# Optimization experiments

Hardware: AMD Instinct MI355X
Metric: run time of the kernel (lower is better)

## Reference

```python
import jax, jax.numpy as jnp
from jax import lax
import numpy as np


def tropical_conv1d(x, w, padding, mode):
    """Tropical semiring conv1d.
    y[b,o,t] = sum_c reduce_k ( x[b,c,t+k] + w[o,c,k] )
    where reduce is min (min-plus) or max (max-plus). Zero padding like nn.Conv1d.
    x: [B, C, L], w: [O, C, K] -> y: [B, O, L + 2p - K + 1]
    """
    if padding:
        x = jnp.pad(x, ((0, 0), (0, 0), (padding, padding)))
    B, C, L = x.shape
    O, _, K = w.shape
    Lo = L - K + 1
    big = jnp.array(np.inf if mode == 'min' else -np.inf, dtype=x.dtype)
    acc0 = jnp.full((B, O, C, Lo), big, dtype=x.dtype)
    red = jnp.minimum if mode == 'min' else jnp.maximum
    wk_all = jnp.moveaxis(w, 2, 0)          # [K, O, C]
    ks = jnp.arange(K)

    def step(acc, inp):
        k, wk = inp
        xs = lax.dynamic_slice_in_dim(x, k, Lo, axis=2)      # [B, C, Lo]
        v = xs[:, None, :, :] + wk[None, :, :, None]          # [B, O, C, Lo]
        return red(acc, v), None

    acc, _ = lax.scan(step, acc0, (ks, wk_all))
    return acc.sum(axis=2)                                    # [B, O, Lo]


def avg_pool1d_2(x):
    # avg_pool1d(kernel=2, stride=2), truncating odd tail like torch
    B, C, L = x.shape
    Lh = L // 2
    return x[..., : Lh * 2].reshape(B, C, Lh, 2).mean(axis=-1)


def setup_inputs() -> dict:
    key = jax.random.key(0)
    ks = jax.random.split(key, 9)
    B, Cin, L = 64, 3, 8192
    linear_size = 32448
    s = lambda k, shape, fan: jax.random.normal(k, shape, dtype=jnp.float32) * (1.0 / np.sqrt(fan))
    return {
        'input': jax.random.normal(ks[0], (B, Cin, L), dtype=jnp.float32),
        'w1': s(ks[1], (6, Cin, 80), Cin * 80),
        'w2': s(ks[2], (16, 6, 3), 6 * 3),
        'fc1_w': s(ks[3], (120, linear_size), linear_size),
        'fc1_b': jnp.zeros((120,), jnp.float32),
        'fc2_w': s(ks[4], (84, 120), 120),
        'fc2_b': jnp.zeros((84,), jnp.float32),
        'fc3_w': s(ks[5], (10, 84), 84),
        'fc3_b': jnp.zeros((10,), jnp.float32),
    }


def reference(input, w1, w2, fc1_w, fc1_b, fc2_w, fc2_b, fc3_w, fc3_b):
    x = tropical_conv1d(input, w1, padding=2, mode='min')   # [B,6,L-75]
    x = avg_pool1d_2(x)
    x = tropical_conv1d(x, w2, padding=0, mode='max')       # [B,16,L2]
    x = avg_pool1d_2(x)
    x = x.reshape(x.shape[0], -1)                            # [B, 16*floor(L2/2)]
    x = jax.nn.relu(x @ fc1_w.T + fc1_b)
    x = jax.nn.relu(x @ fc2_w.T + fc2_b)
    return x @ fc3_w.T + fc3_b
```

## Files before the change

### kernel.cpp

```cpp
#include <hip/hip_runtime.h>

#define BB 64
#define C1 3
#define LIN 8192
#define PAD1 2
#define O1 6
#define KK1 80
#define LP1 4058

#define O2 16
#define KK2 3
#define LP2 2028

#define NFLAT 32448
#define H1 120
#define H2 84
#define NOUT 10

typedef _Float16 h2 __attribute__((ext_vector_type(2)));
typedef _Float16 f16x8 __attribute__((ext_vector_type(8)));
typedef float f32x4 __attribute__((ext_vector_type(4)));
#define BIGH ((_Float16)30000.0f)

__device__ __forceinline__ h2 bch2(float f) { return __builtin_bit_cast(h2, f); }

__global__ __launch_bounds__(256) void k_prep(const float* __restrict__ w1,
                                              float* __restrict__ whb) {
  const int idx = threadIdx.x + blockIdx.x * 256;
  if (idx >= (O1 * C1) * (KK1 / 2)) return;
  const int oc = idx / (KK1 / 2);
  const int m  = idx - oc * (KK1 / 2);
  h2 v;
  v.x = (_Float16)w1[oc * KK1 + 2 * m];
  v.y = (_Float16)w1[oc * KK1 + 2 * m + 1];
  whb[idx] = __builtin_bit_cast(float, v);
}

#define TILE2 127
#define NT12 16
#define DW12 295

__global__ __launch_bounds__(256) void k_conv12(const float* __restrict__ x,
                                                const float* __restrict__ whb,
                                                const float* __restrict__ w2,
                                                _Float16* __restrict__ p2h) {
  __shared__ float AB[C1][2 * DW12 + 2];
  __shared__ float ps[O1][256];
  __shared__ float w2s[O2 * O1 * KK2];
  const int tile = blockIdx.x;
  const int b    = blockIdx.y;
  const int pj0  = 2 * TILE2 * tile;
  const int T0   = 2 * pj0;
  const int tid  = threadIdx.x;

  for (int idx = tid; idx < O2 * O1 * KK2; idx += 256) w2s[idx] = w2[idx];
  for (int q = tid; q < C1 * DW12; q += 256) {
    const int c = q / DW12;
    const int d = q - c * DW12;
    const int E = T0 + 2 * d - PAD1;
    const float* xc = x + ((size_t)b * C1 + c) * LIN;
    float f0 = 0.f, f1 = 0.f, f2 = 0.f;
    if ((unsigned)E < LIN) f0 = xc[E];
    if ((unsigned)(E + 1) < LIN) f1 = xc[E + 1];
    if ((unsigned)(E + 2) < LIN) f2 = xc[E + 2];
    h2 A; A.x = (_Float16)f0; A.y = (_Float16)f1;
    h2 Bv; Bv.x = (_Float16)f1; Bv.y = (_Float16)f2;
    AB[c][2 * d]     = __builtin_bit_cast(float, A);
    AB[c][2 * d + 1] = __builtin_bit_cast(float, Bv);
  }
  __syncthreads();

  const int jj = tid;

  float s0 = 0.f, s1 = 0.f, s2 = 0.f, s3 = 0.f, s4 = 0.f, s5 = 0.f;

#pragma unroll
  for (int c = 0; c < C1; ++c) {
    h2 aA[O1], aB[O1];
#pragma unroll
    for (int o = 0; o < O1; ++o) {
      aA[o].x = BIGH; aA[o].y = BIGH;
      aB[o].x = BIGH; aB[o].y = BIGH;
    }
#pragma unroll 2
    for (int mc = 0; mc < 10; ++mc) {
      float4 xv0 = *(const float4*)&AB[c][2 * (jj + mc * 4)];
      float4 xv1 = *(const float4*)&AB[c][2 * (jj + mc * 4) + 4];
      h2 A0 = bch2(xv0.x), B0 = bch2(xv0.y);
      h2 A1 = bch2(xv0.z), B1 = bch2(xv0.w);
      h2 A2 = bch2(xv1.x), B2 = bch2(xv1.y);
      h2 A3 = bch2(xv1.z), B3 = bch2(xv1.w);
#pragma unroll
      for (int o = 0; o < O1; ++o) {
        float4 wq = *(const float4*)&whb[(o * C1 + c) * (KK1 / 2) + mc * 4];
        h2 w0 = bch2(wq.x), w1v = bch2(wq.y), w2v = bch2(wq.z), w3v = bch2(wq.w);
        aA[o] = __builtin_elementwise_min(aA[o], A0 + w0);
        aB[o] = __builtin_elementwise_min(aB[o], B0 + w0);
        aA[o] = __builtin_elementwise_min(aA[o], A1 + w1v);
        aB[o] = __builtin_elementwise_min(aB[o], B1 + w1v);
        aA[o] = __builtin_elementwise_min(aA[o], A2 + w2v);
        aB[o] = __builtin_elementwise_min(aB[o], B2 + w2v);
        aA[o] = __builtin_elementwise_min(aA[o], A3 + w3v);
        aB[o] = __builtin_elementwise_min(aB[o], B3 + w3v);
      }
    }
    float r[O1];
#pragma unroll
    for (int o = 0; o < O1; ++o)
      r[o] = fminf((float)aA[o].x, (float)aA[o].y) + fminf((float)aB[o].x, (float)aB[o].y);
    s0 += r[0]; s1 += r[1]; s2 += r[2]; s3 += r[3]; s4 += r[4]; s5 += r[5];
  }
  ps[0][jj] = 0.5f * s0;
  ps[1][jj] = 0.5f * s1;
  ps[2][jj] = 0.5f * s2;
  ps[3][jj] = 0.5f * s3;
  ps[4][jj] = 0.5f * s4;
  ps[5][jj] = 0.5f * s5;
  __syncthreads();

  const int j2i = tid & 127;
  const int ot  = tid >> 7;
  const int j2  = TILE2 * tile + j2i;
  if (j2i < TILE2 && j2 < LP2) {
    const int lb = 2 * j2i;
    float xv[O1][4];
#pragma unroll
    for (int c = 0; c < O1; ++c) {
      xv[c][0] = ps[c][lb];     xv[c][1] = ps[c][lb + 1];
      xv[c][2] = ps[c][lb + 2]; xv[c][3] = ps[c][lb + 3];
    }
#pragma unroll
    for (int oi = 0; oi < 8; ++oi) {
      const int o = ot * 8 + oi;
      float s = 0.f;
#pragma unroll
      for (int c = 0; c < O1; ++c) {
        float w0  = w2s[(o * O1 + c) * KK2 + 0];
        float w1v = w2s[(o * O1 + c) * KK2 + 1];
        float w2v = w2s[(o * O1 + c) * KK2 + 2];
        float m0 = fmaxf(fmaxf(xv[c][0] + w0, xv[c][1] + w1v), xv[c][2] + w2v);
        float m1 = fmaxf(fmaxf(xv[c][1] + w0, xv[c][2] + w1v), xv[c][3] + w2v);
        s += m0 + m1;
      }
      p2h[(size_t)b * NFLAT + o * LP2 + j2] = (_Float16)(0.5f * s);
    }
  }
}

#define KC2 64
#define NKC2 507

__global__ __launch_bounds__(256) void k_fc1(const _Float16* __restrict__ p2h,
                                             const float* __restrict__ w,
                                             _Float16* __restrict__ part) {
  __shared__ _Float16 bs[64][KC2];
  const int kc  = blockIdx.x;
  const int k0  = kc * KC2;
  const int tid = threadIdx.x;

#pragma unroll
  for (int r = 0; r < 2; ++r) {
    const int task = tid + 256 * r;
    const int row  = task >> 3;
    const int c4   = task & 7;
    float4 v = *(const float4*)&p2h[(size_t)row * NFLAT + k0 + c4 * 8];
    *(float4*)&bs[row][c4 * 8] = v;
  }
  __syncthreads();

  const int lane = tid & 63;
  const int wid  = tid >> 6;
  const int m_l  = lane & 15;
  const int q    = lane >> 4;
  const int m0   = wid * 32;

  const int rowA0 = m0 + m_l;
  int rowA1 = m0 + 16 + m_l;
  if (rowA1 > H1 - 1) rowA1 = H1 - 1;
  const float* wp0 = w + (size_t)rowA0 * NFLAT + k0 + q * 8;
  const float* wp1 = w + (size_t)rowA1 * NFLAT + k0 + q * 8;

  f32x4 acc[2][4];
#pragma unroll
  for (int t = 0; t < 2; ++t)
#pragma unroll
    for (int nt = 0; nt < 4; ++nt) acc[t][nt] = (f32x4){0.f, 0.f, 0.f, 0.f};

#pragma unroll
  for (int ks = 0; ks < 2; ++ks) {
    float4 a0l = *(const float4*)(wp0 + ks * 32);
    float4 a0h = *(const float4*)(wp0 + ks * 32 + 4);
    float4 a1l = *(const float4*)(wp1 + ks * 32);
    float4 a1h = *(const float4*)(wp1 + ks * 32 + 4);
    f16x8 A0, A1;
    A0[0] = (_Float16)a0l.x; A0[1] = (_Float16)a0l.y;
    A0[2] = (_Float16)a0l.z; A0[3] = (_Float16)a0l.w;
    A0[4] = (_Float16)a0h.x; A0[5] = (_Float16)a0h.y;
    A0[6] = (_Float16)a0h.z; A0[7] = (_Float16)a0h.w;
    A1[0] = (_Float16)a1l.x; A1[1] = (_Float16)a1l.y;
    A1[2] = (_Float16)a1l.z; A1[3] = (_Float16)a1l.w;
    A1[4] = (_Float16)a1h.x; A1[5] = (_Float16)a1h.y;
    A1[6] = (_Float16)a1h.z; A1[7] = (_Float16)a1h.w;
#pragma unroll
    for (int nt = 0; nt < 4; ++nt) {
      f16x8 Bf = *(const f16x8*)&bs[nt * 16 + m_l][ks * 32 + q * 8];
      acc[0][nt] = __builtin_amdgcn_mfma_f32_16x16x32_f16(A0, Bf, acc[0][nt], 0, 0, 0);
      acc[1][nt] = __builtin_amdgcn_mfma_f32_16x16x32_f16(A1, Bf, acc[1][nt], 0, 0, 0);
    }
  }

#pragma unroll
  for (int t = 0; t < 2; ++t)
#pragma unroll
    for (int nt = 0; nt < 4; ++nt)
#pragma unroll
      for (int r = 0; r < 4; ++r) {
        const int i = m0 + t * 16 + q * 4 + r;
        if (i < H1)
          part[((size_t)kc * H1 + i) * 64 + nt * 16 + m_l] = (_Float16)acc[t][nt][r];
      }
}

__global__ __launch_bounds__(1024) void k_h1(const _Float16* __restrict__ part,
                                             const float* __restrict__ fc1_b,
                                             float* __restrict__ h1g) {
  __shared__ float red[1024];
  const int i   = blockIdx.x;
  const int tid = threadIdx.x;
  const int b   = tid & 63;
  const int sub = tid >> 6;
  float acc = 0.f;
  for (int kc = sub; kc < NKC2; kc += 16)
    acc += (float)part[((size_t)kc * H1 + i) * 64 + b];
  red[tid] = acc;
  __syncthreads();
  if (tid < 64) {
    float t = 0.f;
#pragma unroll
    for (int s2 = 0; s2 < 16; ++s2) t += red[b + 64 * s2];
    h1g[i * 64 + b] = fmaxf(t + fc1_b[i], 0.f);
  }
}

__global__ __launch_bounds__(128) void k_head(const float* __restrict__ h1g,
                                              const float* __restrict__ fc2_w,
                                              const float* __restrict__ fc2_b,
                                              const float* __restrict__ fc3_w,
                                              const float* __restrict__ fc3_b,
                                              float* __restrict__ out) {
  __shared__ float h1s[H1];
  __shared__ float h2s[H2];
  const int b = blockIdx.x;
  const int tid = threadIdx.x;
  if (tid < H1) h1s[tid] = h1g[tid * 64 + b];
  __syncthreads();
  if (tid < H2) {
    float s = fc2_b[tid];
#pragma unroll 4
    for (int n = 0; n < H1; ++n) s += h1s[n] * fc2_w[tid * H1 + n];
    h2s[tid] = fmaxf(s, 0.f);
  }
  __syncthreads();
  if (tid < NOUT) {
    float s = fc3_b[tid];
#pragma unroll 4
    for (int n = 0; n < H2; ++n) s += h2s[n] * fc3_w[tid * H2 + n];
    out[b * NOUT + tid] = s;
  }
}

extern "C" void kernel_launch(void* const* d_in, const int* in_sizes, int n_in,
                              void* d_out, int out_size, void* d_ws, size_t ws_size,
                              hipStream_t stream) {
  const float* x     = (const float*)d_in[0];
  const float* w1    = (const float*)d_in[1];
  const float* w2    = (const float*)d_in[2];
  const float* fc1_w = (const float*)d_in[3];
  const float* fc1_b = (const float*)d_in[4];
  const float* fc2_w = (const float*)d_in[5];
  const float* fc2_b = (const float*)d_in[6];
  const float* fc3_w = (const float*)d_in[7];
  const float* fc3_b = (const float*)d_in[8];

  _Float16* p2h  = (_Float16*)d_ws;
  _Float16* part = p2h + (size_t)BB * NFLAT;
  float*    h1g  = (float*)(part + (size_t)NKC2 * H1 * 64);
  float*    whb  = h1g + (size_t)H1 * 64;
  float*    out  = (float*)d_out;

  hipLaunchKernelGGL(k_prep, dim3(3), dim3(256), 0, stream, w1, whb);
  hipLaunchKernelGGL(k_conv12, dim3(NT12, BB), dim3(256), 0, stream, x, whb, w2, p2h);
  hipLaunchKernelGGL(k_fc1, dim3(NKC2), dim3(256), 0, stream, p2h, fc1_w, part);
  hipLaunchKernelGGL(k_h1, dim3(H1), dim3(1024), 0, stream, part, fc1_b, h1g);
  hipLaunchKernelGGL(k_head, dim3(BB), dim3(128), 0, stream, h1g, fc2_w, fc2_b,
                     fc3_w, fc3_b, out);
}
```

Measured before the change: 142.6 us.

## Widen fc1 K-chunks and fuse fc1 reduction with MLP head via last-block counter

The fc1 split-K kernel now uses 128-wide K chunks with 512 threads, one 16-row M tile per wave, and a zero-padded tail chunk. This halves the number of partial-sum slabs written and later reduced. The h1 reduction kernel and the fc2/fc3 head kernel are merged: an atomic counter, reset in k_prep, lets the last finishing block run the head over all 64 batch rows. That removes one launch and its dependency gap, at the cost of running the head serially in a single block.

Measured after the change: 168.7 us. 18.3% more time.

```diff
diff --git a/kernel.cpp b/kernel.cpp
--- a/kernel.cpp
+++ b/kernel.cpp
@@ -25,8 +25,10 @@
 __device__ __forceinline__ h2 bch2(float f) { return __builtin_bit_cast(h2, f); }
 
 __global__ __launch_bounds__(256) void k_prep(const float* __restrict__ w1,
-                                              float* __restrict__ whb) {
+                                              float* __restrict__ whb,
+                                              int* __restrict__ cnt) {
   const int idx = threadIdx.x + blockIdx.x * 256;
+  if (idx == 0) *cnt = 0;
   if (idx >= (O1 * C1) * (KK1 / 2)) return;
   const int oc = idx / (KK1 / 2);
   const int m  = idx - oc * (KK1 / 2);
@@ -147,10 +149,26 @@
   }
 }
 
-#define KC2 64
-#define NKC2 507
-
-__global__ __launch_bounds__(256) void k_fc1(const _Float16* __restrict__ p2h,
+#define KC2 128
+#define NKC2 254
+
+#define FC1_STEP(ks)                                                                     \
+  {                                                                                      \
+    float4 al = *(const float4*)(wp + (ks) * 32);                                        \
+    float4 ah = *(const float4*)(wp + (ks) * 32 + 4);                                    \
+    f16x8 A;                                                                             \
+    A[0] = (_Float16)al.x; A[1] = (_Float16)al.y;                                        \
+    A[2] = (_Float16)al.z; A[3] = (_Float16)al.w;                                        \
+    A[4] = (_Float16)ah.x; A[5] = (_Float16)ah.y;                                        \
+    A[6] = (_Float16)ah.z; A[7] = (_Float16)ah.w;                                        \
+    _Pragma("unroll")                                                                    \
+    for (int nt = 0; nt < 4; ++nt) {                                                     \
+      f16x8 Bf = *(const f16x8*)&bs[nt * 16 + m_l][(ks) * 32 + q * 8];                   \
+      acc[nt] = __builtin_amdgcn_mfma_f32_16x16x32_f16(A, Bf, acc[nt], 0, 0, 0);         \
+    }                                                                                    \
+  }
+
+__global__ __launch_bounds__(512) void k_fc1(const _Float16* __restrict__ p2h,
                                              const float* __restrict__ w,
                                              _Float16* __restrict__ part) {
   __shared__ _Float16 bs[64][KC2];
@@ -160,10 +178,12 @@
 
 #pragma unroll
   for (int r = 0; r < 2; ++r) {
-    const int task = tid + 256 * r;
-    const int row  = task >> 3;
-    const int c4   = task & 7;
-    float4 v = *(const float4*)&p2h[(size_t)row * NFLAT + k0 + c4 * 8];
+    const int task = tid + 512 * r;
+    const int row  = task >> 4;
+    const int c4   = task & 15;
+    const int k    = k0 + c4 * 8;
+    float4 v = {0.f, 0.f, 0.f, 0.f};
+    if (k + 8 <= NFLAT) v = *(const float4*)&p2h[(size_t)row * NFLAT + k];
     *(float4*)&bs[row][c4 * 8] = v;
   }
   __syncthreads();
@@ -172,59 +192,45 @@
   const int wid  = tid >> 6;
   const int m_l  = lane & 15;
   const int q    = lane >> 4;
-  const int m0   = wid * 32;
-
-  const int rowA0 = m0 + m_l;
-  int rowA1 = m0 + 16 + m_l;
-  if (rowA1 > H1 - 1) rowA1 = H1 - 1;
-  const float* wp0 = w + (size_t)rowA0 * NFLAT + k0 + q * 8;
-  const float* wp1 = w + (size_t)rowA1 * NFLAT + k0 + q * 8;
-
-  f32x4 acc[2][4];
-#pragma unroll
-  for (int t = 0; t < 2; ++t)
-#pragma unroll
-    for (int nt = 0; nt < 4; ++nt) acc[t][nt] = (f32x4){0.f, 0.f, 0.f, 0.f};
-
-#pragma unroll
-  for (int ks = 0; ks < 2; ++ks) {
-    float4 a0l = *(const float4*)(wp0 + ks * 32);
-    float4 a0h = *(const float4*)(wp0 + ks * 32 + 4);
-    float4 a1l = *(const float4*)(wp1 + ks * 32);
-    float4 a1h = *(const float4*)(wp1 + ks * 32 + 4);
-    f16x8 A0, A1;
-    A0[0] = (_Float16)a0l.x; A0[1] = (_Float16)a0l.y;
-    A0[2] = (_Float16)a0l.z; A0[3] = (_Float16)a0l.w;
-    A0[4] = (_Float16)a0h.x; A0[5] = (_Float16)a0h.y;
-    A0[6] = (_Float16)a0h.z; A0[7] = (_Float16)a0h.w;
-    A1[0] = (_Float16)a1l.x; A1[1] = (_Float16)a1l.y;
-    A1[2] = (_Float16)a1l.z; A1[3] = (_Float16)a1l.w;
-    A1[4] = (_Float16)a1h.x; A1[5] = (_Float16)a1h.y;
-    A1[6] = (_Float16)a1h.z; A1[7] = (_Float16)a1h.w;
-#pragma unroll
-    for (int nt = 0; nt < 4; ++nt) {
-      f16x8 Bf = *(const f16x8*)&bs[nt * 16 + m_l][ks * 32 + q * 8];
-      acc[0][nt] = __builtin_amdgcn_mfma_f32_16x16x32_f16(A0, Bf, acc[0][nt], 0, 0, 0);
-      acc[1][nt] = __builtin_amdgcn_mfma_f32_16x16x32_f16(A1, Bf, acc[1][nt], 0, 0, 0);
-    }
-  }
-
-#pragma unroll
-  for (int t = 0; t < 2; ++t)
-#pragma unroll
-    for (int nt = 0; nt < 4; ++nt)
-#pragma unroll
-      for (int r = 0; r < 4; ++r) {
-        const int i = m0 + t * 16 + q * 4 + r;
-        if (i < H1)
-          part[((size_t)kc * H1 + i) * 64 + nt * 16 + m_l] = (_Float16)acc[t][nt][r];
-      }
-}
-
-__global__ __launch_bounds__(1024) void k_h1(const _Float16* __restrict__ part,
-                                             const float* __restrict__ fc1_b,
-                                             float* __restrict__ h1g) {
+  const int m0   = wid * 16;
+
+  int rowA = m0 + m_l;
+  if (rowA > H1 - 1) rowA = H1 - 1;
+  const float* wp = w + (size_t)rowA * NFLAT + k0 + q * 8;
+
+  f32x4 acc[4];
+#pragma unroll
+  for (int nt = 0; nt < 4; ++nt) acc[nt] = (f32x4){0.f, 0.f, 0.f, 0.f};
+
+  if (k0 + KC2 <= NFLAT) {
+    FC1_STEP(0) FC1_STEP(1) FC1_STEP(2) FC1_STEP(3)
+  } else {
+    FC1_STEP(0) FC1_STEP(1)
+  }
+
+#pragma unroll
+  for (int nt = 0; nt < 4; ++nt)
+#pragma unroll
+    for (int r = 0; r < 4; ++r) {
+      const int i = m0 + q * 4 + r;
+      if (i < H1)
+        part[((size_t)kc * H1 + i) * 64 + nt * 16 + m_l] = (_Float16)acc[nt][r];
+    }
+}
+
+__global__ __launch_bounds__(1024) void k_h1head(const _Float16* __restrict__ part,
+                                                 const float* __restrict__ fc1_b,
+                                                 const float* __restrict__ fc2_w,
+                                                 const float* __restrict__ fc2_b,
+                                                 const float* __restrict__ fc3_w,
+                                                 const float* __restrict__ fc3_b,
+                                                 float* __restrict__ h1g,
+                                                 int* __restrict__ cnt,
+                                                 float* __restrict__ out) {
   __shared__ float red[1024];
+  __shared__ float h1s[H1 * 64];
+  __shared__ float h2s[H2 * 64];
+  __shared__ int   isLast;
   const int i   = blockIdx.x;
   const int tid = threadIdx.x;
   const int b   = tid & 63;
@@ -240,32 +246,31 @@
     for (int s2 = 0; s2 < 16; ++s2) t += red[b + 64 * s2];
     h1g[i * 64 + b] = fmaxf(t + fc1_b[i], 0.f);
   }
-}
-
-__global__ __launch_bounds__(128) void k_head(const float* __restrict__ h1g,
-                                              const float* __restrict__ fc2_w,
-                                              const float* __restrict__ fc2_b,
-                                              const float* __restrict__ fc3_w,
-                                              const float* __restrict__ fc3_b,
-                                              float* __restrict__ out) {
-  __shared__ float h1s[H1];
-  __shared__ float h2s[H2];
-  const int b = blockIdx.x;
-  const int tid = threadIdx.x;
-  if (tid < H1) h1s[tid] = h1g[tid * 64 + b];
-  __syncthreads();
-  if (tid < H2) {
-    float s = fc2_b[tid];
+  __syncthreads();
+  if (tid == 0) {
+    __threadfence();
+    isLast = (atomicAdd(cnt, 1) == H1 - 1);
+  }
+  __syncthreads();
+  if (!isLast) return;
+
+  __threadfence();
+  for (int t = tid; t < H1 * 64; t += 1024) h1s[t] = h1g[t];
+  __syncthreads();
+  for (int t = tid; t < H2 * 64; t += 1024) {
+    const int bb = t & 63, o = t >> 6;
+    float s = fc2_b[o];
 #pragma unroll 4
-    for (int n = 0; n < H1; ++n) s += h1s[n] * fc2_w[tid * H1 + n];
-    h2s[tid] = fmaxf(s, 0.f);
-  }
-  __syncthreads();
-  if (tid < NOUT) {
-    float s = fc3_b[tid];
+    for (int n = 0; n < H1; ++n) s += h1s[n * 64 + bb] * fc2_w[o * H1 + n];
+    h2s[t] = fmaxf(s, 0.f);
+  }
+  __syncthreads();
+  if (tid < NOUT * 64) {
+    const int bb = tid & 63, o = tid >> 6;
+    float s = fc3_b[o];
 #pragma unroll 4
-    for (int n = 0; n < H2; ++n) s += h2s[n] * fc3_w[tid * H2 + n];
-    out[b * NOUT + tid] = s;
+    for (int n = 0; n < H2; ++n) s += h2s[n * 64 + bb] * fc3_w[o * H2 + n];
+    out[bb * NOUT + o] = s;
   }
 }
 
@@ -286,12 +291,12 @@
   _Float16* part = p2h + (size_t)BB * NFLAT;
   float*    h1g  = (float*)(part + (size_t)NKC2 * H1 * 64);
   float*    whb  = h1g + (size_t)H1 * 64;
+  int*      cnt  = (int*)(whb + 720);
   float*    out  = (float*)d_out;
 
-  hipLaunchKernelGGL(k_prep, dim3(3), dim3(256), 0, stream, w1, whb);
+  hipLaunchKernelGGL(k_prep, dim3(3), dim3(256), 0, stream, w1, whb, cnt);
   hipLaunchKernelGGL(k_conv12, dim3(NT12, BB), dim3(256), 0, stream, x, whb, w2, p2h);
-  hipLaunchKernelGGL(k_fc1, dim3(NKC2), dim3(256), 0, stream, p2h, fc1_w, part);
-  hipLaunchKernelGGL(k_h1, dim3(H1), dim3(1024), 0, stream, part, fc1_b, h1g);
-  hipLaunchKernelGGL(k_head, dim3(BB), dim3(128), 0, stream, h1g, fc2_w, fc2_b,
-                     fc3_w, fc3_b, out);
-}
+  hipLaunchKernelGGL(k_fc1, dim3(NKC2), dim3(512), 0, stream, p2h, fc1_w, part);
+  hipLaunchKernelGGL(k_h1head, dim3(H1), dim3(1024), 0, stream, part, fc1_b, fc2_w,
+                     fc2_b, fc3_w, fc3_b, h1g, cnt, out);
+}
```
